# Performance work log

Measured on AMD Instinct MI355X. Metric: run time of the kernel, lower is better.

Reference implementation:

```python
import jax, jax.numpy as jnp
import numpy as np

H, KVH, DH = 16, 4, 64
DIM = 1024
SCALE_BASE = 4096  # context_len
EPS = 1e-6


def rmsnorm(x, g):
    return x * jax.lax.rsqrt(jnp.mean(x * x, axis=-1, keepdims=True) + EPS) * g


def rope_tables(n, dh, dtype):
    inv_freq = 1.0 / (10000.0 ** (jnp.arange(0, dh, 2, dtype=jnp.float32) / dh))
    t = jnp.arange(n, dtype=jnp.float32) * (SCALE_BASE / n)
    freqs = t[:, None] * inv_freq[None, :]          # [n, dh/2]
    emb = jnp.concatenate([freqs, freqs], axis=-1)  # [n, dh]
    return jnp.cos(emb).astype(dtype), jnp.sin(emb).astype(dtype)


def apply_rope(x, cos, sin):
    # x: [b, h, n, dh]; cos/sin: [n, dh]
    x1, x2 = jnp.split(x, 2, axis=-1)
    rot = jnp.concatenate([-x2, x1], axis=-1)
    return x * cos + rot * sin


def setup_inputs() -> dict:
    key = jax.random.key(0)
    ks = jax.random.split(key, 12)
    B, N = 1, 2048
    std = 0.02
    inp = {
        "x": jax.random.normal(ks[0], (B, N, DIM), jnp.float32),
        "a": jax.random.normal(ks[1], (B, N, DIM), jnp.float32),
        "g_x": jnp.ones((DIM,), jnp.float32),
        "g_a": jnp.ones((DIM,), jnp.float32),
        "Wq_x": jax.random.normal(ks[2], (DIM, H * DH), jnp.float32) * std,
        "Wkv_x": jax.random.normal(ks[3], (DIM, 2 * KVH * DH), jnp.float32) * std,
        "Wq_a": jax.random.normal(ks[4], (DIM, H * DH), jnp.float32) * std,
        "Wkv_a": jax.random.normal(ks[5], (DIM, 2 * KVH * DH), jnp.float32) * std,
        "Wout_x": jax.random.normal(ks[6], (H * DH, DIM), jnp.float32) * std,
        "bout_x": jnp.zeros((DIM,), jnp.float32),
        "Wout_a": jax.random.normal(ks[7], (H * DH, DIM), jnp.float32) * std,
        "bout_a": jnp.zeros((DIM,), jnp.float32),
    }
    return inp


def _split_heads(t, h):
    b, n, hd = t.shape
    return t.reshape(b, n, h, hd // h).transpose(0, 2, 1, 3)  # b h n d


def _stream_qkv(s, g, Wq, Wkv):
    s = rmsnorm(s, g)
    q = _split_heads(s @ Wq, H)                 # [b, H, n, DH]
    kv = s @ Wkv
    k, v = jnp.split(kv, 2, axis=-1)
    k = _split_heads(k, KVH)                    # [b, KVH, n, DH]
    v = _split_heads(v, KVH)
    return q, k, v


def reference(x, a, g_x, g_a, Wq_x, Wkv_x, Wq_a, Wkv_a, Wout_x, bout_x, Wout_a, bout_a):
    B, Nx, _ = x.shape
    Na = a.shape[1]
    scale = DH ** -0.5
    r = H // KVH

    q_x, k_x, v_x = _stream_qkv(x, g_x, Wq_x, Wkv_x)
    q_a, k_a, v_a = _stream_qkv(a, g_a, Wq_a, Wkv_a)

    cos_x, sin_x = rope_tables(Nx, DH, x.dtype)
    cos_a, sin_a = rope_tables(Na, DH, a.dtype)
    q_x, k_x = apply_rope(q_x, cos_x, sin_x), apply_rope(k_x, cos_x, sin_x)
    q_a, k_a = apply_rope(q_a, cos_a, sin_a), apply_rope(k_a, cos_a, sin_a)

    # NOTE: original scales q by dim_head**-0.5 AND sdpa scales again -> 1/DH total
    q_x = q_x * scale
    q_a = q_a * scale

    # GQA expansion: einops 'b h n d -> b (r h) n d' == tile heads
    tile = lambda t: jnp.tile(t, (1, r, 1, 1))
    k_x, v_x, k_a, v_a = tile(k_x), tile(v_x), tile(k_a), tile(v_a)

    # pack [a, x] along seq
    q = jnp.concatenate([q_a, q_x], axis=2)
    k = jnp.concatenate([k_a, k_x], axis=2)
    v = jnp.concatenate([v_a, v_x], axis=2)

    scores = jnp.einsum('bhqd,bhkd->bhqk', q, k) * scale  # sdpa's own scale
    attn = jax.nn.softmax(scores, axis=-1)
    out = jnp.einsum('bhqk,bhkd->bhqd', attn, v)          # [b, H, Na+Nx, DH]

    out_a, out_x = out[:, :, :Na], out[:, :, Na:]
    merge = lambda t: t.transpose(0, 2, 1, 3).reshape(B, -1, H * DH)
    out_x = merge(out_x) @ Wout_x + bout_x
    out_a = merge(out_a) @ Wout_a + bout_a
    return out_x, out_a
```

## Files before the change

### kernel.cpp

```cpp
#include <hip/hip_runtime.h>
#include <hip/hip_bf16.h>
#include <stdint.h>
#include <math.h>


#define NSEQ 2048
#define NJ   4096
#define DIMM 1024

typedef __attribute__((ext_vector_type(4))) float f32x4;
typedef __attribute__((ext_vector_type(8))) short bf16x8;
typedef __attribute__((ext_vector_type(4))) short bf16x4;

__device__ __forceinline__ unsigned short f2bf(float f) {
  union { float f; uint32_t u; } v; v.f = f;
  return (unsigned short)((v.u + 0x7FFFu + ((v.u >> 16) & 1u)) >> 16);
}

__device__ __forceinline__ uint32_t pack2bf(float a, float b) {
  __hip_bfloat162 h = __float22bfloat162_rn(float2{a, b});
  union { __hip_bfloat162 h; uint32_t u; } c; c.h = h;
  return c.u;
}

#if defined(__has_builtin)
#if __has_builtin(__builtin_amdgcn_exp2f)
#define FAST_EXP2(x) __builtin_amdgcn_exp2f(x)
#endif
#endif
#ifndef FAST_EXP2
#define FAST_EXP2(x) exp2f(x)
#endif

__device__ __forceinline__ void glds16(const void* g, void* l) {
  __builtin_amdgcn_global_load_lds(
      (const __attribute__((address_space(1))) unsigned int*)g,
      (__attribute__((address_space(3))) unsigned int*)l, 16, 0, 0);
}

__global__ __launch_bounds__(256) void prep_kernel(
    const float* __restrict__ xa, const float* __restrict__ xx,
    const float* __restrict__ ga, const float* __restrict__ gx,
    const float* __restrict__ wqa, const float* __restrict__ wqx,
    const float* __restrict__ wkva, const float* __restrict__ wkvx,
    const float* __restrict__ woa, const float* __restrict__ wox,
    unsigned short* __restrict__ XN, unsigned short* __restrict__ WQT,
    unsigned short* __restrict__ WKVT, unsigned short* __restrict__ WOT,
    float* __restrict__ cosT, float* __restrict__ sinT) {
  __shared__ float tile[32][33];
  __shared__ float red[4];
  int bid = blockIdx.x, t = threadIdx.x;
  if (bid < 256) {
    int idx = bid * 256 + t;
    int pos = idx >> 5, i = idx & 31;
    double inv = pow(10000.0, -(double)i / 32.0);
    double ang = (double)(2 * pos) * inv;
    cosT[idx] = (float)cos(ang);
    sinT[idx] = (float)sin(ang);
  } else if (bid < 6400) {
    int b = bid - 256;
    int z = b >> 10, yx = b & 1023;
    int n0 = (yx >> 5) * 32, k0 = (yx & 31) * 32;
    int s = z & 1, ty = z >> 1;
    int N = (ty == 1) ? 512 : 1024;
    if (n0 >= N) return;
    const float* src = (z == 0) ? wqa : (z == 1) ? wqx : (z == 2) ? wkva
                     : (z == 3) ? wkvx : (z == 4) ? woa : wox;
    unsigned short* dst = (ty == 0) ? WQT + (size_t)s * 1024 * 1024
                        : (ty == 1) ? WKVT + (size_t)s * 512 * 1024
                                    : WOT + (size_t)s * 1024 * 1024;
    int r = t >> 3, c4 = (t & 7) * 4;
    f32x4 v = *(const f32x4*)(src + (size_t)(k0 + r) * N + n0 + c4);
    tile[r][c4 + 0] = v.x; tile[r][c4 + 1] = v.y;
    tile[r][c4 + 2] = v.z; tile[r][c4 + 3] = v.w;
    __syncthreads();
    int nn = t >> 3, kk = (t & 7) * 4;
    bf16x4 o;
    o.x = (short)f2bf(tile[kk + 0][nn]);
    o.y = (short)f2bf(tile[kk + 1][nn]);
    o.z = (short)f2bf(tile[kk + 2][nn]);
    o.w = (short)f2bf(tile[kk + 3][nn]);
    *(bf16x4*)(dst + (size_t)(n0 + nn) * 1024 + k0 + kk) = o;
  } else {
    int b = bid - 6400;
    int s = b >> 11, row = b & 2047;
    const float* src = (s == 0 ? xa : xx) + (size_t)row * DIMM;
    const float* g = (s == 0 ? ga : gx);
    f32x4 v = *(const f32x4*)(src + t * 4);
    float ss = v.x * v.x + v.y * v.y + v.z * v.z + v.w * v.w;
#pragma unroll
    for (int o = 32; o > 0; o >>= 1) ss += __shfl_xor(ss, o, 64);
    if ((t & 63) == 0) red[t >> 6] = ss;
    __syncthreads();
    float tot = red[0] + red[1] + red[2] + red[3];
    float rs = rsqrtf(tot * (1.0f / DIMM) + 1e-6f);
    f32x4 gv = *(const f32x4*)(g + t * 4);
    bf16x4 o;
    o.x = (short)f2bf(v.x * rs * gv.x);
    o.y = (short)f2bf(v.y * rs * gv.y);
    o.z = (short)f2bf(v.z * rs * gv.z);
    o.w = (short)f2bf(v.w * rs * gv.w);
    *(bf16x4*)(XN + ((size_t)s * NSEQ + row) * DIMM + t * 4) = o;
  }
}

__device__ __forceinline__ void gemm64_mainloop(
    const unsigned short* __restrict__ Ag, const unsigned short* __restrict__ Bg,
    unsigned short* As, unsigned short* Bs, f32x4 acc[2][4]) {
  int t = threadIdx.x;
  int lane = t & 63, wid = t >> 6;
  int wm = (wid >> 1) * 32, wn = (wid & 1) * 64;
  int l15 = lane & 15, quad = lane >> 4;
  int srow = t >> 2, sko = (t & 3) * 8;
  const unsigned short* ga = Ag + (size_t)srow * 1024 + sko;
  const unsigned short* gb = Bg + (size_t)srow * 1024 + sko;
  unsigned short* la = As + t * 8;
  unsigned short* lb = Bs + t * 8;
#pragma unroll
  for (int mi = 0; mi < 2; ++mi)
#pragma unroll
    for (int j = 0; j < 4; ++j) acc[mi][j] = (f32x4){0.f, 0.f, 0.f, 0.f};
  for (int kt = 0; kt < 32; ++kt) {
    int k0 = kt * 32;
    __syncthreads();
    glds16(ga + k0, la);
    glds16(gb + k0, lb);
    glds16(gb + 64 * 1024 + k0, lb + 2048);
    __syncthreads();
    bf16x8 af[2], bfr[4];
#pragma unroll
    for (int mi = 0; mi < 2; ++mi)
      af[mi] = *(const bf16x8*)(As + (wm + mi * 16 + l15) * 32 + quad * 8);
#pragma unroll
    for (int j = 0; j < 4; ++j)
      bfr[j] = *(const bf16x8*)(Bs + (wn + j * 16 + l15) * 32 + quad * 8);
#pragma unroll
    for (int mi = 0; mi < 2; ++mi)
#pragma unroll
      for (int j = 0; j < 4; ++j)
        acc[mi][j] = __builtin_amdgcn_mfma_f32_16x16x32_bf16(af[mi], bfr[j],
                                                             acc[mi][j], 0, 0, 0);
  }
}

__global__ __launch_bounds__(256) void gemm_qkv_kernel(
    const unsigned short* __restrict__ XN, const unsigned short* __restrict__ WQT,
    const unsigned short* __restrict__ WKVT, const float* __restrict__ cosT,
    const float* __restrict__ sinT, unsigned short* __restrict__ QB,
    unsigned short* __restrict__ KB, unsigned short* __restrict__ VT) {
  __shared__ unsigned short As[64 * 32], Bs[128 * 32];
  int n0 = blockIdx.x * 128, m0 = blockIdx.y * 64;
  int s = (m0 >= 2048) ? 1 : 0;
  const unsigned short* Ag = XN + (size_t)m0 * 1024;
  const unsigned short* Bg = (n0 < 1024)
      ? WQT + (size_t)s * 1024 * 1024 + (size_t)n0 * 1024
      : WKVT + (size_t)s * 512 * 1024 + (size_t)(n0 - 1024) * 1024;
  f32x4 acc[2][4];
  gemm64_mainloop(Ag, Bg, As, Bs, acc);
  int t = threadIdx.x, lane = t & 63, wid = t >> 6;
  int wm = (wid >> 1) * 32, wn = (wid & 1) * 64;
  int l15 = lane & 15, quad = lane >> 4;
  int coln = n0 + wn;
  if (coln < 1280) {
    bool isq = coln < 1024;
    float sc = isq ? (1.4426950408889634f / 64.0f) : 1.0f;
    unsigned short* dstBase;
    if (isq) dstBase = QB + (size_t)(coln >> 6) * NJ * 64;
    else     dstBase = KB + (size_t)((coln - 1024) >> 6) * NJ * 64;
#pragma unroll
    for (int mi = 0; mi < 2; ++mi)
#pragma unroll
      for (int r = 0; r < 4; ++r) {
        int jr = m0 + wm + mi * 16 + quad * 4 + r;
        int pos = jr & 2047;
#pragma unroll
        for (int jp = 0; jp < 2; ++jp) {
          int i = jp * 16 + l15;
          float c = cosT[pos * 32 + i], sn = sinT[pos * 32 + i];
          float x1 = acc[mi][jp][r], x2 = acc[mi][jp + 2][r];
          dstBase[(size_t)jr * 64 + jp * 16 + l15]      = f2bf((x1 * c - x2 * sn) * sc);
          dstBase[(size_t)jr * 64 + 32 + jp * 16 + l15] = f2bf((x2 * c + x1 * sn) * sc);
        }
      }
  } else {
    int cvb = coln - 1280;
#pragma unroll
    for (int mi = 0; mi < 2; ++mi)
#pragma unroll
      for (int j = 0; j < 4; ++j) {
        int d = cvb + j * 16 + l15;
        int jr0 = m0 + wm + mi * 16 + quad * 4;
        union { bf16x4 v; uint32_t u[2]; } pv;
        pv.u[0] = pack2bf(acc[mi][j][0], acc[mi][j][1]);
        pv.u[1] = pack2bf(acc[mi][j][2], acc[mi][j][3]);
        *(bf16x4*)(VT + (size_t)d * NJ + jr0) = pv.v;
      }
  }
}

__global__ __launch_bounds__(256, 2) void attn_kernel(
    const unsigned short* __restrict__ QB, const unsigned short* __restrict__ KB,
    const unsigned short* __restrict__ VT, unsigned short* __restrict__ AT) {
  __shared__ __align__(16) unsigned short Ks[4][4096];
  __shared__ __align__(16) unsigned short Vs[4][4096];
  int h = blockIdx.y, qt = blockIdx.x;
  int hk = h & 3;
  int t = threadIdx.x, lane = t & 63, w = t >> 6;
  int l15 = lane & 15, quad = lane >> 4;
  int qsel = w >> 1, ksel = w & 1;
  int q0 = qt * 128 + qsel * 64;
  bf16x8 qf[4][2];
#pragma unroll
  for (int mi = 0; mi < 4; ++mi) {
    const unsigned short* qp = QB + ((size_t)h * NJ + q0 + mi * 16 + l15) * 64;
    qf[mi][0] = *(const bf16x8*)(qp + quad * 8);
    qf[mi][1] = *(const bf16x8*)(qp + 32 + quad * 8);
  }
  f32x4 oT[4][4];
  f32x4 oL[4];
#pragma unroll
  for (int mi = 0; mi < 4; ++mi) {
    oL[mi] = (f32x4){0.f, 0.f, 0.f, 0.f};
#pragma unroll
    for (int db = 0; db < 4; ++db) oT[mi][db] = (f32x4){0.f, 0.f, 0.f, 0.f};
  }
  bf16x8 vone;
  {
    short one = (l15 == 0) ? (short)0x3F80 : (short)0;
    vone = (bf16x8){one, one, one, one, one, one, one, one};
  }
  const unsigned short* Kg = KB + (size_t)hk * NJ * 64;
  const unsigned short* Vg = VT + (size_t)hk * 64 * NJ;
  int r1 = t >> 3, cx = t & 7;
  int e1 = r1 & 7;
  int c1 = cx ^ e1;
  int gk1 = 32 * (r1 >> 5) + 8 * ((r1 >> 2) & 3) + 4 * ((r1 >> 4) & 1) + (r1 & 3);
  int r2 = r1 + 32;
  int gk2 = 32 * (r2 >> 5) + 8 * ((r2 >> 2) & 3) + 4 * ((r2 >> 4) & 1) + (r2 & 3);
  const unsigned short* sK1 = Kg + (size_t)gk1 * 64 + c1 * 8;
  const unsigned short* sK2 = Kg + (size_t)gk2 * 64 + c1 * 8;
  const unsigned short* sV1 = Vg + (size_t)r1 * NJ + c1 * 8;
  const unsigned short* sV2 = Vg + (size_t)r2 * NJ + c1 * 8;
  int e = l15 & 7;
  int co0 = (quad ^ e) * 8;
  int co1 = ((4 + quad) ^ e) * 8;
  int cov = (((ksel << 2) | quad) ^ e) * 8;
  const unsigned short* kf0p = &Ks[0][(2 * ksel * 16 + l15) * 64] + co0;
  const unsigned short* kf0q = &Ks[0][(2 * ksel * 16 + l15) * 64] + co1;
  const unsigned short* kf1p = kf0p + 16 * 64;
  const unsigned short* kf1q = kf0q + 16 * 64;
  const unsigned short* vap0 = &Vs[0][(0 * 16 + l15) * 64] + cov;
  const unsigned short* vap1 = &Vs[0][(1 * 16 + l15) * 64] + cov;
  const unsigned short* vap2 = &Vs[0][(2 * 16 + l15) * 64] + cov;
  const unsigned short* vap3 = &Vs[0][(3 * 16 + l15) * 64] + cov;

  f32x4 sxA[4][2], sxB[4][2];
  bf16x8 pb[4];

#define STAGE(S, T) do {                                                   \
    size_t ko_ = (size_t)(T) * 4096;                                       \
    int vo_ = (T) * 64;                                                    \
    glds16(sK1 + ko_, &Ks[S][0] + t * 8);                                  \
    glds16(sK2 + ko_, &Ks[S][2048] + t * 8);                               \
    glds16(sV1 + vo_, &Vs[S][0] + t * 8);                                  \
    glds16(sV2 + vo_, &Vs[S][2048] + t * 8);                               \
  } while (0)

#define QK4(S, SX) do {                                                    \
    bf16x8 k00 = *(const bf16x8*)(kf0p + (S) * 4096);                      \
    bf16x8 k01 = *(const bf16x8*)(kf0q + (S) * 4096);                      \
    bf16x8 k10 = *(const bf16x8*)(kf1p + (S) * 4096);                      \
    bf16x8 k11 = *(const bf16x8*)(kf1q + (S) * 4096);                      \
    _Pragma("unroll")                                                      \
    for (int mi = 0; mi < 4; ++mi) {                                       \
      f32x4 z0 = (f32x4){0.f, 0.f, 0.f, 0.f};                              \
      z0 = __builtin_amdgcn_mfma_f32_16x16x32_bf16(k00, qf[mi][0], z0, 0, 0, 0); \
      z0 = __builtin_amdgcn_mfma_f32_16x16x32_bf16(k01, qf[mi][1], z0, 0, 0, 0); \
      (SX)[mi][0] = z0;                                                    \
      f32x4 z1 = (f32x4){0.f, 0.f, 0.f, 0.f};                              \
      z1 = __builtin_amdgcn_mfma_f32_16x16x32_bf16(k10, qf[mi][0], z1, 0, 0, 0); \
      z1 = __builtin_amdgcn_mfma_f32_16x16x32_bf16(k11, qf[mi][1], z1, 0, 0, 0); \
      (SX)[mi][1] = z1;                                                    \
    }                                                                      \
  } while (0)

#define PHASE_A(SQ, SXN, SXP) do {                                         \
    bf16x8 k00 = *(const bf16x8*)(kf0p + (SQ) * 4096);                     \
    bf16x8 k01 = *(const bf16x8*)(kf0q + (SQ) * 4096);                     \
    bf16x8 k10 = *(const bf16x8*)(kf1p + (SQ) * 4096);                     \
    bf16x8 k11 = *(const bf16x8*)(kf1q + (SQ) * 4096);                     \
    _Pragma("unroll")                                                      \
    for (int mi = 0; mi < 4; ++mi) {                                       \
      f32x4 z0 = (f32x4){0.f, 0.f, 0.f, 0.f};                              \
      z0 = __builtin_amdgcn_mfma_f32_16x16x32_bf16(k00, qf[mi][0], z0, 0, 0, 0); \
      z0 = __builtin_amdgcn_mfma_f32_16x16x32_bf16(k01, qf[mi][1], z0, 0, 0, 0); \
      (SXN)[mi][0] = z0;                                                   \
      f32x4 z1 = (f32x4){0.f, 0.f, 0.f, 0.f};                              \
      z1 = __builtin_amdgcn_mfma_f32_16x16x32_bf16(k10, qf[mi][0], z1, 0, 0, 0); \
      z1 = __builtin_amdgcn_mfma_f32_16x16x32_bf16(k11, qf[mi][1], z1, 0, 0, 0); \
      (SXN)[mi][1] = z1;                                                   \
      union { bf16x8 v; uint32_t u[4]; } pk_;                              \
      pk_.u[0] = pack2bf(FAST_EXP2((SXP)[mi][0][0]), FAST_EXP2((SXP)[mi][0][1])); \
      pk_.u[1] = pack2bf(FAST_EXP2((SXP)[mi][0][2]), FAST_EXP2((SXP)[mi][0][3])); \
      pk_.u[2] = pack2bf(FAST_EXP2((SXP)[mi][1][0]), FAST_EXP2((SXP)[mi][1][1])); \
      pk_.u[3] = pack2bf(FAST_EXP2((SXP)[mi][1][2]), FAST_EXP2((SXP)[mi][1][3])); \
      pb[mi] = pk_.v;                                                      \
    }                                                                      \
  } while (0)

#define PHASE_B(SP) do {                                                   \
    __builtin_amdgcn_s_setprio(1);                                         \
    {                                                                      \
      bf16x8 va0 = *(const bf16x8*)(vap0 + (SP) * 4096);                   \
      bf16x8 va1 = *(const bf16x8*)(vap1 + (SP) * 4096);                   \
      bf16x8 va2 = *(const bf16x8*)(vap2 + (SP) * 4096);                   \
      bf16x8 va3 = *(const bf16x8*)(vap3 + (SP) * 4096);                   \
      _Pragma("unroll")                                                    \
      for (int mi = 0; mi < 4; ++mi) {                                     \
        oT[mi][0] = __builtin_amdgcn_mfma_f32_16x16x32_bf16(va0, pb[mi], oT[mi][0], 0, 0, 0); \
        oT[mi][1] = __builtin_amdgcn_mfma_f32_16x16x32_bf16(va1, pb[mi], oT[mi][1], 0, 0, 0); \
        oT[mi][2] = __builtin_amdgcn_mfma_f32_16x16x32_bf16(va2, pb[mi], oT[mi][2], 0, 0, 0); \
        oT[mi][3] = __builtin_amdgcn_mfma_f32_16x16x32_bf16(va3, pb[mi], oT[mi][3], 0, 0, 0); \
        oL[mi] = __builtin_amdgcn_mfma_f32_16x16x32_bf16(vone, pb[mi], oL[mi], 0, 0, 0); \
      }                                                                    \
    }                                                                      \
    __builtin_amdgcn_s_setprio(0);                                         \
  } while (0)

  STAGE(0, 0);
  STAGE(1, 1);
  __syncthreads();
  QK4(0, sxA);
  for (int P = 0; P < 16; ++P) {
    int tb = 4 * P;
    STAGE(2, (tb + 2) & 63);
    PHASE_A(1, sxB, sxA);
    PHASE_B(0);
    __syncthreads();
    STAGE(3, (tb + 3) & 63);
    PHASE_A(2, sxA, sxB);
    PHASE_B(1);
    __syncthreads();
    STAGE(0, (tb + 4) & 63);
    PHASE_A(3, sxB, sxA);
    PHASE_B(2);
    __syncthreads();
    STAGE(1, (tb + 5) & 63);
    PHASE_A(0, sxA, sxB);
    PHASE_B(3);
    __syncthreads();
  }
#undef STAGE
#undef QK4
#undef PHASE_A
#undef PHASE_B

  float ls[4];
#pragma unroll
  for (int mi = 0; mi < 4; ++mi) {
    float s = oL[mi][0];
    s += __shfl_xor(s, 16, 64);
    s += __shfl_xor(s, 32, 64);
    ls[mi] = s;
  }
  float* xb = (qsel == 0) ? (float*)&Ks[0][0] : (float*)&Vs[0][0];
  float* xl = xb + 64 * 68;
  if (ksel == 1) {
    f32x4* dst = (f32x4*)xb + (size_t)lane * 17;
#pragma unroll
    for (int mi = 0; mi < 4; ++mi)
#pragma unroll
      for (int db = 0; db < 4; ++db) dst[mi * 4 + db] = oT[mi][db];
    float* dl = xl + lane * 4;
#pragma unroll
    for (int mi = 0; mi < 4; ++mi) dl[mi] = ls[mi];
  }
  __syncthreads();
  if (ksel == 0) {
    const f32x4* src = (const f32x4*)xb + (size_t)lane * 17;
    const float* sl = xl + lane * 4;
#pragma unroll
    for (int mi = 0; mi < 4; ++mi) {
      float inv = 1.0f / (ls[mi] + sl[mi]);
      int qrow = q0 + mi * 16 + l15;
#pragma unroll
      for (int db = 0; db < 4; ++db) {
        f32x4 o = oT[mi][db] + src[mi * 4 + db];
        union { bf16x4 v; uint32_t u[2]; } ov;
        ov.u[0] = pack2bf(o[0] * inv, o[1] * inv);
        ov.u[1] = pack2bf(o[2] * inv, o[3] * inv);
        *(bf16x4*)(AT + (size_t)qrow * DIMM + h * 64 + db * 16 + quad * 4) = ov.v;
      }
    }
  }
}

__global__ __launch_bounds__(256) void gemm_out_kernel(
    const unsigned short* __restrict__ AT, const unsigned short* __restrict__ WOT,
    const float* __restrict__ ba, const float* __restrict__ bx,
    float* __restrict__ out) {
  __shared__ unsigned short As[64 * 32], Bs[128 * 32];
  int n0 = blockIdx.x * 128, m0 = blockIdx.y * 64;
  int s = (m0 >= 2048) ? 1 : 0;
  const unsigned short* Ag = AT + (size_t)m0 * 1024;
  const unsigned short* Bg = WOT + (size_t)s * 1024 * 1024 + (size_t)n0 * 1024;
  f32x4 acc[2][4];
  gemm64_mainloop(Ag, Bg, As, Bs, acc);
  int t = threadIdx.x, lane = t & 63, wid = t >> 6;
  int wm = (wid >> 1) * 32, wn = (wid & 1) * 64;
  int l15 = lane & 15, quad = lane >> 4;
  const float* bias = s ? bx : ba;
  float* obase = s ? (out + (size_t)(m0 - 2048) * 1024)
                   : (out + (size_t)2048 * 1024 + (size_t)m0 * 1024);
#pragma unroll
  for (int mi = 0; mi < 2; ++mi)
#pragma unroll
    for (int r = 0; r < 4; ++r) {
      int row = wm + mi * 16 + quad * 4 + r;
#pragma unroll
      for (int j = 0; j < 4; ++j) {
        int col = n0 + wn + j * 16 + l15;
        obase[(size_t)row * 1024 + col] = acc[mi][j][r] + bias[col];
      }
    }
}

extern "C" void kernel_launch(void* const* d_in, const int* in_sizes, int n_in,
                              void* d_out, int out_size, void* d_ws, size_t ws_size,
                              hipStream_t stream) {
  const float* x      = (const float*)d_in[0];
  const float* a      = (const float*)d_in[1];
  const float* g_x    = (const float*)d_in[2];
  const float* g_a    = (const float*)d_in[3];
  const float* Wq_x   = (const float*)d_in[4];
  const float* Wkv_x  = (const float*)d_in[5];
  const float* Wq_a   = (const float*)d_in[6];
  const float* Wkv_a  = (const float*)d_in[7];
  const float* Wout_x = (const float*)d_in[8];
  const float* bout_x = (const float*)d_in[9];
  const float* Wout_a = (const float*)d_in[10];
  const float* bout_a = (const float*)d_in[11];
  float* out = (float*)d_out;

  char* ws = (char*)d_ws;
  const size_t MB = 1024 * 1024;
  unsigned short* XN   = (unsigned short*)(ws);
  unsigned short* WQT  = (unsigned short*)(ws + 8 * MB);
  unsigned short* WKVT = (unsigned short*)(ws + 12 * MB);
  unsigned short* WOT  = (unsigned short*)(ws + 14 * MB);
  unsigned short* QB   = (unsigned short*)(ws + 18 * MB);
  unsigned short* KB   = (unsigned short*)(ws + 26 * MB);
  unsigned short* VT   = (unsigned short*)(ws + 28 * MB);
  float* cosT          = (float*)(ws + 30 * MB);
  float* sinT          = (float*)(ws + 30 * MB + 262144);
  unsigned short* AT   = XN;

  prep_kernel<<<dim3(10496), dim3(256), 0, stream>>>(
      a, x, g_a, g_x, Wq_a, Wq_x, Wkv_a, Wkv_x, Wout_a, Wout_x,
      XN, WQT, WKVT, WOT, cosT, sinT);
  gemm_qkv_kernel<<<dim3(12, 64), dim3(256), 0, stream>>>(
      XN, WQT, WKVT, cosT, sinT, QB, KB, VT);
  attn_kernel<<<dim3(32, 16), dim3(256), 0, stream>>>(QB, KB, VT, AT);
  gemm_out_kernel<<<dim3(8, 64), dim3(256), 0, stream>>>(
      AT, WOT, bout_a, bout_x, out);
}
```

Measured before the change: 217.2 us.

## Multi-buffer GEMM mainloop and restructure attention loop to interleave exp with PV

The shared GEMM mainloop for the QKV and output projections now uses a 4-stage LDS ring. Two k-tiles are prefetched ahead and processed in pairs, so there are two barriers per four k-tiles instead of two per tile. The attention inner loop is reorganized to process two key tiles per barrier: the exp/pack of the second tile is interleaved with the PV MFMAs of the first, using double-buffered P registers. This raises LDS use per GEMM block fourfold and register pressure in attention, which may reduce occupancy.

```diff
diff --git a/kernel.cpp b/kernel.cpp
--- a/kernel.cpp
+++ b/kernel.cpp
@@ -120,27 +120,46 @@
   for (int mi = 0; mi < 2; ++mi)
 #pragma unroll
     for (int j = 0; j < 4; ++j) acc[mi][j] = (f32x4){0.f, 0.f, 0.f, 0.f};
-  for (int kt = 0; kt < 32; ++kt) {
-    int k0 = kt * 32;
+
+#define GQ_STAGE(S, KT) do {                                               \
+    int k0_ = (KT) * 32;                                                   \
+    glds16(ga + k0_, la + (S) * 2048);                                     \
+    glds16(gb + k0_, lb + (S) * 4096);                                     \
+    glds16(gb + 64 * 1024 + k0_, lb + (S) * 4096 + 2048);                  \
+  } while (0)
+
+#define GQ_COMP(S) do {                                                    \
+    bf16x8 af[2], bfr[4];                                                  \
+    _Pragma("unroll")                                                      \
+    for (int mi = 0; mi < 2; ++mi)                                         \
+      af[mi] = *(const bf16x8*)(As + (S) * 2048 + (wm + mi * 16 + l15) * 32 + quad * 8); \
+    _Pragma("unroll")                                                      \
+    for (int j = 0; j < 4; ++j)                                            \
+      bfr[j] = *(const bf16x8*)(Bs + (S) * 4096 + (wn + j * 16 + l15) * 32 + quad * 8); \
+    _Pragma("unroll")                                                      \
+    for (int mi = 0; mi < 2; ++mi)                                         \
+      _Pragma("unroll")                                                    \
+      for (int j = 0; j < 4; ++j)                                          \
+        acc[mi][j] = __builtin_amdgcn_mfma_f32_16x16x32_bf16(af[mi], bfr[j], acc[mi][j], 0, 0, 0); \
+  } while (0)
+
+  GQ_STAGE(0, 0);
+  GQ_STAGE(1, 1);
+  __syncthreads();
+  for (int kq = 0; kq < 32; kq += 4) {
+    GQ_STAGE(2, (kq + 2) & 31);
+    GQ_STAGE(3, (kq + 3) & 31);
+    GQ_COMP(0);
+    GQ_COMP(1);
     __syncthreads();
-    glds16(ga + k0, la);
-    glds16(gb + k0, lb);
-    glds16(gb + 64 * 1024 + k0, lb + 2048);
+    GQ_STAGE(0, (kq + 4) & 31);
+    GQ_STAGE(1, (kq + 5) & 31);
+    GQ_COMP(2);
+    GQ_COMP(3);
     __syncthreads();
-    bf16x8 af[2], bfr[4];
-#pragma unroll
-    for (int mi = 0; mi < 2; ++mi)
-      af[mi] = *(const bf16x8*)(As + (wm + mi * 16 + l15) * 32 + quad * 8);
-#pragma unroll
-    for (int j = 0; j < 4; ++j)
-      bfr[j] = *(const bf16x8*)(Bs + (wn + j * 16 + l15) * 32 + quad * 8);
-#pragma unroll
-    for (int mi = 0; mi < 2; ++mi)
-#pragma unroll
-      for (int j = 0; j < 4; ++j)
-        acc[mi][j] = __builtin_amdgcn_mfma_f32_16x16x32_bf16(af[mi], bfr[j],
-                                                             acc[mi][j], 0, 0, 0);
-  }
+  }
+#undef GQ_STAGE
+#undef GQ_COMP
 }
 
 __global__ __launch_bounds__(256) void gemm_qkv_kernel(
@@ -148,7 +167,7 @@
     const unsigned short* __restrict__ WKVT, const float* __restrict__ cosT,
     const float* __restrict__ sinT, unsigned short* __restrict__ QB,
     unsigned short* __restrict__ KB, unsigned short* __restrict__ VT) {
-  __shared__ unsigned short As[64 * 32], Bs[128 * 32];
+  __shared__ unsigned short As[4 * 2048], Bs[4 * 4096];
   int n0 = blockIdx.x * 128, m0 = blockIdx.y * 64;
   int s = (m0 >= 2048) ? 1 : 0;
   const unsigned short* Ag = XN + (size_t)m0 * 1024;
@@ -255,7 +274,7 @@
   const unsigned short* vap3 = &Vs[0][(3 * 16 + l15) * 64] + cov;
 
   f32x4 sxA[4][2], sxB[4][2];
-  bf16x8 pb[4];
+  bf16x8 pbA[4], pbB[4];
 
 #define STAGE(S, T) do {                                                   \
     size_t ko_ = (size_t)(T) * 4096;                                       \
@@ -284,7 +303,7 @@
     }                                                                      \
   } while (0)
 
-#define PHASE_A(SQ, SXN, SXP) do {                                         \
+#define PHASE_A(SQ, SXN, SXP, PB) do {                                     \
     bf16x8 k00 = *(const bf16x8*)(kf0p + (SQ) * 4096);                     \
     bf16x8 k01 = *(const bf16x8*)(kf0q + (SQ) * 4096);                     \
     bf16x8 k10 = *(const bf16x8*)(kf1p + (SQ) * 4096);                     \
@@ -304,11 +323,32 @@
       pk_.u[1] = pack2bf(FAST_EXP2((SXP)[mi][0][2]), FAST_EXP2((SXP)[mi][0][3])); \
       pk_.u[2] = pack2bf(FAST_EXP2((SXP)[mi][1][0]), FAST_EXP2((SXP)[mi][1][1])); \
       pk_.u[3] = pack2bf(FAST_EXP2((SXP)[mi][1][2]), FAST_EXP2((SXP)[mi][1][3])); \
-      pb[mi] = pk_.v;                                                      \
+      (PB)[mi] = pk_.v;                                                    \
     }                                                                      \
   } while (0)
 
-#define PHASE_B(SP) do {                                                   \
+#define PHASE_C(SP, PB, SX, PBN) do {                                      \
+    bf16x8 va0 = *(const bf16x8*)(vap0 + (SP) * 4096);                     \
+    bf16x8 va1 = *(const bf16x8*)(vap1 + (SP) * 4096);                     \
+    bf16x8 va2 = *(const bf16x8*)(vap2 + (SP) * 4096);                     \
+    bf16x8 va3 = *(const bf16x8*)(vap3 + (SP) * 4096);                     \
+    _Pragma("unroll")                                                      \
+    for (int mi = 0; mi < 4; ++mi) {                                       \
+      oT[mi][0] = __builtin_amdgcn_mfma_f32_16x16x32_bf16(va0, (PB)[mi], oT[mi][0], 0, 0, 0); \
+      oT[mi][1] = __builtin_amdgcn_mfma_f32_16x16x32_bf16(va1, (PB)[mi], oT[mi][1], 0, 0, 0); \
+      oT[mi][2] = __builtin_amdgcn_mfma_f32_16x16x32_bf16(va2, (PB)[mi], oT[mi][2], 0, 0, 0); \
+      oT[mi][3] = __builtin_amdgcn_mfma_f32_16x16x32_bf16(va3, (PB)[mi], oT[mi][3], 0, 0, 0); \
+      oL[mi]    = __builtin_amdgcn_mfma_f32_16x16x32_bf16(vone, (PB)[mi], oL[mi], 0, 0, 0); \
+      union { bf16x8 v; uint32_t u[4]; } pk_;                              \
+      pk_.u[0] = pack2bf(FAST_EXP2((SX)[mi][0][0]), FAST_EXP2((SX)[mi][0][1])); \
+      pk_.u[1] = pack2bf(FAST_EXP2((SX)[mi][0][2]), FAST_EXP2((SX)[mi][0][3])); \
+      pk_.u[2] = pack2bf(FAST_EXP2((SX)[mi][1][0]), FAST_EXP2((SX)[mi][1][1])); \
+      pk_.u[3] = pack2bf(FAST_EXP2((SX)[mi][1][2]), FAST_EXP2((SX)[mi][1][3])); \
+      (PBN)[mi] = pk_.v;                                                   \
+    }                                                                      \
+  } while (0)
+
+#define PHASE_B(SP, PB) do {                                               \
     __builtin_amdgcn_s_setprio(1);                                         \
     {                                                                      \
       bf16x8 va0 = *(const bf16x8*)(vap0 + (SP) * 4096);                   \
@@ -317,11 +357,11 @@
       bf16x8 va3 = *(const bf16x8*)(vap3 + (SP) * 4096);                   \
       _Pragma("unroll")                                                    \
       for (int mi = 0; mi < 4; ++mi) {                                     \
-        oT[mi][0] = __builtin_amdgcn_mfma_f32_16x16x32_bf16(va0, pb[mi], oT[mi][0], 0, 0, 0); \
-        oT[mi][1] = __builtin_amdgcn_mfma_f32_16x16x32_bf16(va1, pb[mi], oT[mi][1], 0, 0, 0); \
-        oT[mi][2] = __builtin_amdgcn_mfma_f32_16x16x32_bf16(va2, pb[mi], oT[mi][2], 0, 0, 0); \
-        oT[mi][3] = __builtin_amdgcn_mfma_f32_16x16x32_bf16(va3, pb[mi], oT[mi][3], 0, 0, 0); \
-        oL[mi] = __builtin_amdgcn_mfma_f32_16x16x32_bf16(vone, pb[mi], oL[mi], 0, 0, 0); \
+        oT[mi][0] = __builtin_amdgcn_mfma_f32_16x16x32_bf16(va0, (PB)[mi], oT[mi][0], 0, 0, 0); \
+        oT[mi][1] = __builtin_amdgcn_mfma_f32_16x16x32_bf16(va1, (PB)[mi], oT[mi][1], 0, 0, 0); \
+        oT[mi][2] = __builtin_amdgcn_mfma_f32_16x16x32_bf16(va2, (PB)[mi], oT[mi][2], 0, 0, 0); \
+        oT[mi][3] = __builtin_amdgcn_mfma_f32_16x16x32_bf16(va3, (PB)[mi], oT[mi][3], 0, 0, 0); \
+        oL[mi]    = __builtin_amdgcn_mfma_f32_16x16x32_bf16(vone, (PB)[mi], oL[mi], 0, 0, 0); \
       }                                                                    \
     }                                                                      \
     __builtin_amdgcn_s_setprio(0);                                         \
@@ -330,29 +370,27 @@
   STAGE(0, 0);
   STAGE(1, 1);
   __syncthreads();
-  QK4(0, sxA);
   for (int P = 0; P < 16; ++P) {
     int tb = 4 * P;
     STAGE(2, (tb + 2) & 63);
-    PHASE_A(1, sxB, sxA);
-    PHASE_B(0);
-    __syncthreads();
     STAGE(3, (tb + 3) & 63);
-    PHASE_A(2, sxA, sxB);
-    PHASE_B(1);
+    QK4(0, sxA);
+    PHASE_A(1, sxB, sxA, pbA);
+    PHASE_C(0, pbA, sxB, pbB);
+    PHASE_B(1, pbB);
     __syncthreads();
     STAGE(0, (tb + 4) & 63);
-    PHASE_A(3, sxB, sxA);
-    PHASE_B(2);
-    __syncthreads();
     STAGE(1, (tb + 5) & 63);
-    PHASE_A(0, sxA, sxB);
-    PHASE_B(3);
+    QK4(2, sxA);
+    PHASE_A(3, sxB, sxA, pbA);
+    PHASE_C(2, pbA, sxB, pbB);
+    PHASE_B(3, pbB);
     __syncthreads();
   }
 #undef STAGE
 #undef QK4
 #undef PHASE_A
+#undef PHASE_C
 #undef PHASE_B
 
   float ls[4];
@@ -399,7 +437,7 @@
     const unsigned short* __restrict__ AT, const unsigned short* __restrict__ WOT,
     const float* __restrict__ ba, const float* __restrict__ bx,
     float* __restrict__ out) {
-  __shared__ unsigned short As[64 * 32], Bs[128 * 32];
+  __shared__ unsigned short As[4 * 2048], Bs[4 * 4096];
   int n0 = blockIdx.x * 128, m0 = blockIdx.y * 64;
   int s = (m0 >= 2048) ? 1 : 0;
   const unsigned short* Ag = AT + (size_t)m0 * 1024;
```

Result: no change. 218.3 us (+0.5%).
